# Kernel tuning notes

Hardware: AMD Instinct MI355X
Metric: run time of the kernel (lower is better)

Reference implementation:

```python
import jax, jax.numpy as jnp
import numpy as np

B, S, D, H = 2, 4096, 512, 8
HD = D // H
SCALE = float(np.sqrt(HD))


def setup_inputs() -> dict:
    key = jax.random.key(0)
    ks = jax.random.split(key, 11)
    std = 1.0 / np.sqrt(D)
    inp = {
        "query": jax.random.normal(ks[0], (B, S, D), jnp.float32),
        "key": jax.random.normal(ks[1], (B, S, D), jnp.float32),
        "value": jax.random.normal(ks[2], (B, S, D), jnp.float32),
        "Wq": jax.random.normal(ks[3], (D, D), jnp.float32) * std,
        "bq": jnp.zeros((D,), jnp.float32),
        "Wk": jax.random.normal(ks[4], (D, D), jnp.float32) * std,
        "bk": jnp.zeros((D,), jnp.float32),
        "Wv": jax.random.normal(ks[5], (D, D), jnp.float32) * std,
        "bv": jnp.zeros((D,), jnp.float32),
        "Wo": jax.random.normal(ks[6], (D, D), jnp.float32) * std,
        "bo": jnp.zeros((D,), jnp.float32),
    }
    return inp


def reference(query, key, value, Wq, bq, Wk, bk, Wv, bv, Wo, bo):
    # Linear projections, split into heads: [B, H, S, HD]
    def proj(x, W, b):
        y = jnp.einsum('bsd,df->bsf', x, W) + b
        return y.reshape(B, -1, H, HD).transpose(0, 2, 1, 3)

    Q = proj(query, Wq, bq)
    K = proj(key, Wk, bk)
    V = proj(value, Wv, bv)

    # Full [B, H, S, S] score matrix (faithful to the naive original)
    scores = jnp.einsum('bhqd,bhkd->bhqk', Q, K) / SCALE
    attn = jax.nn.softmax(scores, axis=-1)  # dropout = identity in eval
    attended = jnp.einsum('bhqk,bhkd->bhqd', attn, V)
    attended = attended.transpose(0, 2, 1, 3).reshape(B, -1, D)
    return jnp.einsum('bsd,df->bsf', attended, Wo) + bo
```

## Files before the change

kernel.cpp:

```cpp
#include <hip/hip_runtime.h>

typedef short short8 __attribute__((ext_vector_type(8)));
typedef short short4v __attribute__((ext_vector_type(4)));
typedef float f32x4 __attribute__((ext_vector_type(4)));
typedef float f32x16 __attribute__((ext_vector_type(16)));
typedef unsigned uint2v __attribute__((ext_vector_type(2)));

typedef __attribute__((address_space(1))) void gvoid;
typedef __attribute__((address_space(3))) void lvoid;

#define DEV static __device__ __forceinline__

constexpr int Dm = 512;
constexpr int Sm = 4096;
constexpr int Hh = 8;
constexpr long NTe = (long)2 * Sm * Dm;

#define QSCALE 0.18033688011112042f

DEV short f2bf(float f) {
  union { float f; unsigned u; } v; v.f = f;
  unsigned r = v.u + 0x7FFFu + ((v.u >> 16) & 1u);
  return (short)(r >> 16);
}

DEV float exp2_fast(float x) {
#if __has_builtin(__builtin_amdgcn_exp2f)
  return __builtin_amdgcn_exp2f(x);
#else
  return exp2f(x);
#endif
}

DEV float max3f(float a, float b, float c) { return fmaxf(fmaxf(a, b), c); }

DEV unsigned cvt_pk_bf16(float lo, float hi) {
  unsigned r;
  asm("v_cvt_pk_bf16_f32 %0, %1, %2" : "=v"(r) : "v"(lo), "v"(hi));
  return r;
}

DEV uint2v pl32swap(unsigned a, unsigned b) {
  return __builtin_amdgcn_permlane32_swap(a, b, false, false);
}
DEV float swap_max(float x) { return fmaxf(x, __shfl_xor(x, 32, 64)); }
DEV float swap_add(float x) { return x + __shfl_xor(x, 32, 64); }

DEV void async16(const void* g, void* l) {
  __builtin_amdgcn_global_load_lds((gvoid*)g, (lvoid*)l, 16, 0, 0);
}

__global__ __launch_bounds__(256) void cast_qkv(
    const float* __restrict__ q, const float* __restrict__ k,
    const float* __restrict__ v, short* __restrict__ xq,
    short* __restrict__ xk, short* __restrict__ xv) {
  int t = blockIdx.y;
  const float* src = (t == 0) ? q : (t == 1) ? k : v;
  short* dst = (t == 0) ? xq : (t == 1) ? xk : xv;
  long i = (long)(blockIdx.x * 256 + threadIdx.x) * 4;
  float4 f = *(const float4*)(src + i);
  short4v o;
  o[0] = f2bf(f.x); o[1] = f2bf(f.y); o[2] = f2bf(f.z); o[3] = f2bf(f.w);
  *(short4v*)(dst + i) = o;
}

__global__ __launch_bounds__(256) void wtrans(
    const float* __restrict__ wq, const float* __restrict__ wk,
    const float* __restrict__ wv, const float* __restrict__ wo,
    short* __restrict__ wt) {
  __shared__ short T[64 * 72];
  const int tid = threadIdx.x;
  const int n0 = blockIdx.x * 64, k0 = blockIdx.y * 64, w = blockIdx.z;
  const float* W = (w == 0) ? wq : (w == 1) ? wk : (w == 2) ? wv : wo;
  for (int t = 0; t < 4; ++t) {
    int flat = t * 256 + tid;
    int r = flat >> 4, c4 = flat & 15;
    float4 f = *(const float4*)(W + (k0 + r) * 512 + n0 + c4 * 4);
    T[(c4 * 4 + 0) * 72 + r] = f2bf(f.x);
    T[(c4 * 4 + 1) * 72 + r] = f2bf(f.y);
    T[(c4 * 4 + 2) * 72 + r] = f2bf(f.z);
    T[(c4 * 4 + 3) * 72 + r] = f2bf(f.w);
  }
  __syncthreads();
  for (int t = 0; t < 2; ++t) {
    int flat = t * 256 + tid;
    int r = flat >> 3, c = flat & 7;
    short8 v = *(const short8*)(T + r * 72 + c * 8);
    *(short8*)(wt + ((long)w << 18) + (n0 + r) * 512 + k0 + c * 8) = v;
  }
}

__global__ __launch_bounds__(256) void vtrans(
    const short* __restrict__ V, short* __restrict__ VT) {
  __shared__ short T[64 * 72];
  const int tid = threadIdx.x;
  const int s0 = blockIdx.x * 64, d0 = blockIdx.y * 64, b = blockIdx.z;
  for (int t = 0; t < 2; ++t) {
    int flat = t * 256 + tid;
    int sl = flat >> 3, c = flat & 7;
    short8 v = *(const short8*)(V + ((long)b * Sm + s0 + sl) * Dm + d0 + c * 8);
    for (int j = 0; j < 8; ++j) T[(c * 8 + j) * 72 + sl] = v[j];
  }
  __syncthreads();
  for (int t = 0; t < 2; ++t) {
    int flat = t * 256 + tid;
    int dl = flat >> 3, c = flat & 7;
    short8 v = *(const short8*)(T + dl * 72 + c * 8);
    *(short8*)(VT + ((long)b * Dm + d0 + dl) * Sm + s0 + c * 8) = v;
  }
}

template <bool OUT_BF16>
DEV void gemm_body(const short* __restrict__ A, const short* __restrict__ Bt,
                   const float* __restrict__ bias, float scale,
                   void* __restrict__ Yv, short* As, short* Bs) {
  constexpr int K = 512, N = 512, BK = 64;
  const int tid = threadIdx.x, lane = tid & 63, w = tid >> 6;
  const int lm = lane & 15, lg = lane >> 4;
  const int wr = w >> 1, wc = w & 1;
  const long bm = (long)blockIdx.y * 128;
  const long bn = (long)blockIdx.x * 128;
  f32x4 zero = {0.f, 0.f, 0.f, 0.f};
  f32x4 acc[4][4];
  for (int m = 0; m < 4; ++m)
    for (int n = 0; n < 4; ++n) acc[m][n] = zero;
  for (int k0 = 0; k0 < K; k0 += BK) {
    __syncthreads();
    for (int t = 0; t < 4; ++t) {
      int flat = t * 256 + tid;
      int row = flat >> 3, c = flat & 7;
      async16(A + (bm + row) * K + k0 + ((c ^ (row & 7)) * 8), As + flat * 8);
    }
    for (int t = 0; t < 4; ++t) {
      int flat = t * 256 + tid;
      int row = flat >> 3, c = flat & 7;
      async16(Bt + (bn + row) * K + k0 + ((c ^ (row & 7)) * 8), Bs + flat * 8);
    }
    __syncthreads();
    for (int kk = 0; kk < 2; ++kk) {
      short8 a[4], b[4];
      for (int m = 0; m < 4; ++m)
        a[m] = *(const short8*)(As + (wr * 64 + m * 16 + lm) * BK +
                                ((kk * 4 + lg) ^ (lm & 7)) * 8);
      for (int n = 0; n < 4; ++n)
        b[n] = *(const short8*)(Bs + (wc * 64 + n * 16 + lm) * BK +
                                ((kk * 4 + lg) ^ (lm & 7)) * 8);
      for (int m = 0; m < 4; ++m)
        for (int n = 0; n < 4; ++n)
          acc[m][n] = __builtin_amdgcn_mfma_f32_16x16x32_bf16(a[m], b[n], acc[m][n], 0, 0, 0);
    }
  }
  for (int m = 0; m < 4; ++m)
    for (int n = 0; n < 4; ++n) {
      long row0 = bm + wr * 64 + m * 16 + lg * 4;
      int col = (int)bn + wc * 64 + n * 16 + lm;
      float bb = bias[col];
      for (int j = 0; j < 4; ++j) {
        float val = (acc[m][n][j] + bb) * scale;
        if (OUT_BF16)
          ((short*)Yv)[(row0 + j) * N + col] = f2bf(val);
        else
          ((float*)Yv)[(row0 + j) * N + col] = val;
      }
    }
}

__global__ __launch_bounds__(256) void gemm_proj(
    const short* __restrict__ Xq, const short* __restrict__ Xk,
    const short* __restrict__ Xv, const short* __restrict__ Wt,
    const float* __restrict__ bq, const float* __restrict__ bk,
    const float* __restrict__ bv, short* __restrict__ Qb,
    short* __restrict__ Kb, short* __restrict__ Vb) {
  __shared__ short As[128 * 64];
  __shared__ short Bs[128 * 64];
  int z = blockIdx.z;
  const short* A = (z == 0) ? Xq : (z == 1) ? Xk : Xv;
  const short* Bt = Wt + (long)z * 512 * 512;
  const float* bias = (z == 0) ? bq : (z == 1) ? bk : bv;
  short* Y = (z == 0) ? Qb : (z == 1) ? Kb : Vb;
  float scale = (z == 0) ? QSCALE : 1.f;
  gemm_body<true>(A, Bt, bias, scale, Y, As, Bs);
}

__global__ __launch_bounds__(256) void gemm_out(
    const short* __restrict__ A, const short* __restrict__ Bt,
    const float* __restrict__ bias, float* __restrict__ Y) {
  __shared__ short As[128 * 64];
  __shared__ short Bs[128 * 64];
  gemm_body<false>(A, Bt, bias, 1.f, Y, As, Bs);
}

template <int NSPLIT>
__global__ __launch_bounds__(256) void attn(
    const short* __restrict__ Qb, const short* __restrict__ Kb,
    const short* __restrict__ VTb, float* __restrict__ Op0,
    float* __restrict__ OpRest, float2* __restrict__ Ml) {
  __shared__ short Ks[2][64 * 64];
  __shared__ short Vt[2][64 * 64];
  const int tid = threadIdx.x, lane = tid & 63, w = tid >> 6;
  const int q32 = lane & 31, l5 = lane >> 5;
  const int bh = blockIdx.y, b = bh >> 3, h = bh & 7;
  const int z = blockIdx.z;
  constexpr int KVLEN = Sm / NSPLIT;
  const int kvbase = z * KVLEN;
  const long baseQ = (long)b * Sm * Dm + h * 64;
  const long baseVT = ((long)b * Dm + h * 64) * Sm;
  const int q0w = blockIdx.x * 128 + w * 32;

  short8 qf[4];
#pragma unroll
  for (int ks = 0; ks < 4; ++ks)
    qf[ks] = *(const short8*)(Qb + baseQ + (long)(q0w + q32) * Dm + ks * 16 + l5 * 8);

  f32x16 o0, o1;
#pragma unroll
  for (int r = 0; r < 16; ++r) { o0[r] = 0.f; o1[r] = 0.f; }
  float mrun = -1e30f, lrun = 0.f;

  const int r0 = tid >> 3, c0 = tid & 7;
  const int r1 = 32 + (tid >> 3);
  const short* gk0 = Kb + baseQ + (long)(kvbase + r0) * Dm + (c0 ^ (r0 & 7)) * 8;
  const short* gk1 = Kb + baseQ + (long)(kvbase + r1) * Dm + (c0 ^ (r1 & 7)) * 8;
  const short* gv0 = VTb + baseVT + (long)r0 * Sm + kvbase + (c0 ^ (r0 & 7)) * 8;
  const short* gv1 = VTb + baseVT + (long)r1 * Sm + kvbase + (c0 ^ (r1 & 7)) * 8;
  const int l0 = tid * 8, l1 = (256 + tid) * 8;

  async16(gk0, &Ks[0][l0]); async16(gk1, &Ks[0][l1]);
  async16(gv0, &Vt[0][l0]); async16(gv1, &Vt[0][l1]);
  gk0 += 64 * Dm; gk1 += 64 * Dm; gv0 += 64; gv1 += 64;
  __syncthreads();

  const int cxor = q32 & 7;

  constexpr int NTILES = KVLEN / 64;
  for (int it = 0; it < NTILES; ++it) {
    const int cur = it & 1;
    if (it + 1 < NTILES) {
      async16(gk0, &Ks[cur ^ 1][l0]); async16(gk1, &Ks[cur ^ 1][l1]);
      async16(gv0, &Vt[cur ^ 1][l0]); async16(gv1, &Vt[cur ^ 1][l1]);
      gk0 += 64 * Dm; gk1 += 64 * Dm; gv0 += 64; gv1 += 64;
    }

    f32x16 sc0, sc1;
#pragma unroll
    for (int r = 0; r < 16; ++r) { sc0[r] = 0.f; sc1[r] = 0.f; }
    __builtin_amdgcn_s_setprio(1);
#pragma unroll
    for (int ks = 0; ks < 4; ++ks) {
      int cx = (2 * ks + l5) ^ cxor;
      short8 kf0 = *(const short8*)(&Ks[cur][q32 * 64 + cx * 8]);
      short8 kf1 = *(const short8*)(&Ks[cur][(32 + q32) * 64 + cx * 8]);
      sc0 = __builtin_amdgcn_mfma_f32_32x32x16_bf16(kf0, qf[ks], sc0, 0, 0, 0);
      sc1 = __builtin_amdgcn_mfma_f32_32x32x16_bf16(kf1, qf[ks], sc1, 0, 0, 0);
    }
    __builtin_amdgcn_s_setprio(0);

    float t1 = max3f(sc0[0], sc0[1], sc0[2]);
    float t2 = max3f(sc0[3], sc0[4], sc0[5]);
    float t3 = max3f(sc0[6], sc0[7], sc0[8]);
    float t4 = max3f(sc0[9], sc0[10], sc0[11]);
    float t5 = max3f(sc0[12], sc0[13], sc0[14]);
    float ma = max3f(max3f(t1, t2, t3), max3f(t4, t5, sc0[15]), sc1[0]);
    t1 = max3f(sc1[1], sc1[2], sc1[3]);
    t2 = max3f(sc1[4], sc1[5], sc1[6]);
    t3 = max3f(sc1[7], sc1[8], sc1[9]);
    t4 = max3f(sc1[10], sc1[11], sc1[12]);
    t5 = max3f(sc1[13], sc1[14], sc1[15]);
    float tmax = fmaxf(ma, max3f(max3f(t1, t2, t3), t4, t5));
    tmax = swap_max(tmax);

    if (__any(tmax > mrun + 8.f)) {
      float mi = fmaxf(mrun, tmax);
      float cc = exp2_fast(mrun - mi);
      mrun = mi;
      lrun *= cc;
#pragma unroll
      for (int r = 0; r < 16; ++r) {
        float ccr = __shfl(cc, ((r & 3) + 8 * (r >> 2)) + 4 * l5, 32);
        o0[r] *= ccr;
        o1[r] *= ccr;
      }
    }

    float la = 0.f, lb = 0.f;
#pragma unroll
    for (int r = 0; r < 16; ++r) {
      sc0[r] = exp2_fast(sc0[r] - mrun); la += sc0[r];
      sc1[r] = exp2_fast(sc1[r] - mrun); lb += sc1[r];
    }
    lrun += la + lb;

    __builtin_amdgcn_s_setprio(1);
#pragma unroll
    for (int kc = 0; kc < 4; ++kc) {
      const f32x16& sch = (kc < 2) ? sc0 : sc1;
      const int bb = 8 * (kc & 1);
      unsigned A = cvt_pk_bf16(sch[bb + 0], sch[bb + 1]);
      unsigned B = cvt_pk_bf16(sch[bb + 2], sch[bb + 3]);
      unsigned C = cvt_pk_bf16(sch[bb + 4], sch[bb + 5]);
      unsigned D = cvt_pk_bf16(sch[bb + 6], sch[bb + 7]);
      uint2v rac = pl32swap(A, C);
      uint2v rbd = pl32swap(B, D);
      union { unsigned u[4]; short8 s; } pu;
      pu.u[0] = rac[0]; pu.u[1] = rbd[0]; pu.u[2] = rac[1]; pu.u[3] = rbd[1];
      int cx = (2 * kc + l5) ^ cxor;
      short8 vf0 = *(const short8*)(&Vt[cur][q32 * 64 + cx * 8]);
      short8 vf1 = *(const short8*)(&Vt[cur][(32 + q32) * 64 + cx * 8]);
      o0 = __builtin_amdgcn_mfma_f32_32x32x16_bf16(pu.s, vf0, o0, 0, 0, 0);
      o1 = __builtin_amdgcn_mfma_f32_32x32x16_bf16(pu.s, vf1, o1, 0, 0, 0);
    }
    __builtin_amdgcn_s_setprio(0);
    __syncthreads();
  }

  lrun = swap_add(lrun);

  float* Op = (z == 0) ? Op0 : OpRest + (long)(z - 1) * NTe;
#pragma unroll
  for (int r = 0; r < 16; ++r) {
    int q = (r & 3) + 8 * (r >> 2) + 4 * l5;
    long rowoff = baseQ + (long)(q0w + q) * Dm;
    Op[rowoff + q32] = o0[r];
    Op[rowoff + 32 + q32] = o1[r];
  }
  if (l5 == 0) {
    float2 ml; ml.x = mrun; ml.y = lrun;
    Ml[(long)(z * 16 + bh) * Sm + q0w + q32] = ml;
  }
}

template <int NSPLIT>
__global__ __launch_bounds__(256) void mergeN(
    const float* __restrict__ Op0, const float* __restrict__ OpRest,
    const float2* __restrict__ Ml, short* __restrict__ Ob) {
  long idx = (long)blockIdx.x * 256 + threadIdx.x;
  long row = idx >> 6;
  int c8 = (int)(idx & 63);
  int col = c8 * 8;
  int h = col >> 6;
  int b = (int)(row >> 12);
  int s = (int)(row & 4095);
  int bh = b * 8 + h;
  float2 ml[NSPLIT];
  float M = -3e38f;
#pragma unroll
  for (int z = 0; z < NSPLIT; ++z) {
    ml[z] = Ml[(long)(z * 16 + bh) * Sm + s];
    M = fmaxf(M, ml[z].x);
  }
  float wz[NSPLIT], den = 0.f;
#pragma unroll
  for (int z = 0; z < NSPLIT; ++z) {
    wz[z] = exp2_fast(ml[z].x - M);
    den += ml[z].y * wz[z];
  }
  float inv = 1.0f / den;
  long off = row * 512 + col;
  float acc[8];
#pragma unroll
  for (int i = 0; i < 8; ++i) acc[i] = 0.f;
#pragma unroll
  for (int z = 0; z < NSPLIT; ++z) {
    const float* Op = (z == 0) ? Op0 : OpRest + (long)(z - 1) * NTe;
    float4 a0 = *(const float4*)(Op + off);
    float4 a1 = *(const float4*)(Op + off + 4);
    acc[0] += a0.x * wz[z]; acc[1] += a0.y * wz[z];
    acc[2] += a0.z * wz[z]; acc[3] += a0.w * wz[z];
    acc[4] += a1.x * wz[z]; acc[5] += a1.y * wz[z];
    acc[6] += a1.z * wz[z]; acc[7] += a1.w * wz[z];
  }
  short8 o;
#pragma unroll
  for (int i = 0; i < 8; ++i) o[i] = f2bf(acc[i] * inv);
  *(short8*)(Ob + off) = o;
}

extern "C" void kernel_launch(void* const* d_in, const int* in_sizes, int n_in,
                              void* d_out, int out_size, void* d_ws, size_t ws_size,
                              hipStream_t stream) {
  const float* query = (const float*)d_in[0];
  const float* key_  = (const float*)d_in[1];
  const float* value = (const float*)d_in[2];
  const float* Wq = (const float*)d_in[3]; const float* bq = (const float*)d_in[4];
  const float* Wk = (const float*)d_in[5]; const float* bk = (const float*)d_in[6];
  const float* Wv = (const float*)d_in[7]; const float* bv = (const float*)d_in[8];
  const float* Wo = (const float*)d_in[9]; const float* bo = (const float*)d_in[10];

  short* Xq = (short*)d_ws;
  short* Xk = Xq + NTe;
  short* Xv = Xk + NTe;
  short* Wt = Xv + NTe;
  short* Qb = Wt + 4 * 512 * 512;
  short* Kb = Qb + NTe;
  short* Vb = Kb + NTe;
  short* VT = Xv;
  float* Op0 = (float*)d_ws;
  float* OpRest = (float*)(Vb + NTe);
  short* Ob = Vb;

  const size_t base_bytes = (size_t)(6 * NTe + 4 * 512 * 512) * 2;
  const size_t need4 = base_bytes + 3 * (size_t)NTe * 4 + (size_t)4 * 16 * Sm * 8;
  const int nsplit = (ws_size >= need4) ? 4 : 2;
  float2* Ml = (float2*)(OpRest + (size_t)(nsplit - 1) * NTe);

  cast_qkv<<<dim3(4096, 3), 256, 0, stream>>>(query, key_, value, Xq, Xk, Xv);
  wtrans<<<dim3(8, 8, 4), 256, 0, stream>>>(Wq, Wk, Wv, Wo, Wt);

  gemm_proj<<<dim3(4, 64, 3), 256, 0, stream>>>(Xq, Xk, Xv, Wt, bq, bk, bv,
                                                Qb, Kb, Vb);

  vtrans<<<dim3(Sm / 64, Dm / 64, 2), 256, 0, stream>>>(Vb, VT);

  if (nsplit == 4) {
    attn<4><<<dim3(Sm / 128, 2 * Hh, 4), 256, 0, stream>>>(Qb, Kb, VT, Op0,
                                                           OpRest, Ml);
    mergeN<4><<<dim3((2 * Sm * 512 / 8) / 256), 256, 0, stream>>>(Op0, OpRest,
                                                                  Ml, Ob);
  } else {
    attn<2><<<dim3(Sm / 128, 2 * Hh, 2), 256, 0, stream>>>(Qb, Kb, VT, Op0,
                                                           OpRest, Ml);
    mergeN<2><<<dim3((2 * Sm * 512 / 8) / 256), 256, 0, stream>>>(Op0, OpRest,
                                                                  Ml, Ob);
  }

  gemm_out<<<dim3(4, 64), 256, 0, stream>>>(Ob, Wt + 3L * 512 * 512, bo,
                                            (float*)d_out);
}
```

Before: 184.9 us.

## Store split-KV partials in bf16, widen LDS swizzle, split row-sum accumulators

The attention kernel now writes its unnormalised split-KV partial outputs as bf16 instead of fp32, and the merge kernel reads them back as short8 and converts to float. This halves the partial-output write and read traffic between attention and merge, and shrinks the workspace needed for the 4-way split. It also changes the LDS XOR swizzle to mix bit 3 of the row into the column, aiming to cut bank conflicts in the GEMM and attention tiles. The exp row-sum is split into four partial accumulators to shorten the dependency chain. Rounding the partials to bf16 before the merge adds some numerical error.

```diff
diff --git a/kernel.cpp b/kernel.cpp
--- a/kernel.cpp
+++ b/kernel.cpp
@@ -22,6 +22,12 @@
   union { float f; unsigned u; } v; v.f = f;
   unsigned r = v.u + 0x7FFFu + ((v.u >> 16) & 1u);
   return (short)(r >> 16);
+}
+
+DEV float bf2f(short s) {
+  unsigned u = ((unsigned)(unsigned short)s) << 16;
+  union { unsigned u; float f; } v; v.u = u;
+  return v.f;
 }
 
 DEV float exp2_fast(float x) {
@@ -39,6 +45,8 @@
   asm("v_cvt_pk_bf16_f32 %0, %1, %2" : "=v"(r) : "v"(lo), "v"(hi));
   return r;
 }
+
+DEV int fr(int r) { return (r & 7) ^ (((r >> 3) & 1) << 2); }
 
 DEV uint2v pl32swap(unsigned a, unsigned b) {
   return __builtin_amdgcn_permlane32_swap(a, b, false, false);
@@ -129,22 +137,22 @@
     for (int t = 0; t < 4; ++t) {
       int flat = t * 256 + tid;
       int row = flat >> 3, c = flat & 7;
-      async16(A + (bm + row) * K + k0 + ((c ^ (row & 7)) * 8), As + flat * 8);
+      async16(A + (bm + row) * K + k0 + ((c ^ fr(row)) * 8), As + flat * 8);
     }
     for (int t = 0; t < 4; ++t) {
       int flat = t * 256 + tid;
       int row = flat >> 3, c = flat & 7;
-      async16(Bt + (bn + row) * K + k0 + ((c ^ (row & 7)) * 8), Bs + flat * 8);
+      async16(Bt + (bn + row) * K + k0 + ((c ^ fr(row)) * 8), Bs + flat * 8);
     }
     __syncthreads();
     for (int kk = 0; kk < 2; ++kk) {
       short8 a[4], b[4];
       for (int m = 0; m < 4; ++m)
         a[m] = *(const short8*)(As + (wr * 64 + m * 16 + lm) * BK +
-                                ((kk * 4 + lg) ^ (lm & 7)) * 8);
+                                ((kk * 4 + lg) ^ fr(lm)) * 8);
       for (int n = 0; n < 4; ++n)
         b[n] = *(const short8*)(Bs + (wc * 64 + n * 16 + lm) * BK +
-                                ((kk * 4 + lg) ^ (lm & 7)) * 8);
+                                ((kk * 4 + lg) ^ fr(lm)) * 8);
       for (int m = 0; m < 4; ++m)
         for (int n = 0; n < 4; ++n)
           acc[m][n] = __builtin_amdgcn_mfma_f32_16x16x32_bf16(a[m], b[n], acc[m][n], 0, 0, 0);
@@ -193,8 +201,8 @@
 template <int NSPLIT>
 __global__ __launch_bounds__(256) void attn(
     const short* __restrict__ Qb, const short* __restrict__ Kb,
-    const short* __restrict__ VTb, float* __restrict__ Op0,
-    float* __restrict__ OpRest, float2* __restrict__ Ml) {
+    const short* __restrict__ VTb, short* __restrict__ Op0,
+    short* __restrict__ OpRest, float2* __restrict__ Ml) {
   __shared__ short Ks[2][64 * 64];
   __shared__ short Vt[2][64 * 64];
   const int tid = threadIdx.x, lane = tid & 63, w = tid >> 6;
@@ -219,10 +227,10 @@
 
   const int r0 = tid >> 3, c0 = tid & 7;
   const int r1 = 32 + (tid >> 3);
-  const short* gk0 = Kb + baseQ + (long)(kvbase + r0) * Dm + (c0 ^ (r0 & 7)) * 8;
-  const short* gk1 = Kb + baseQ + (long)(kvbase + r1) * Dm + (c0 ^ (r1 & 7)) * 8;
-  const short* gv0 = VTb + baseVT + (long)r0 * Sm + kvbase + (c0 ^ (r0 & 7)) * 8;
-  const short* gv1 = VTb + baseVT + (long)r1 * Sm + kvbase + (c0 ^ (r1 & 7)) * 8;
+  const short* gk0 = Kb + baseQ + (long)(kvbase + r0) * Dm + (c0 ^ fr(r0)) * 8;
+  const short* gk1 = Kb + baseQ + (long)(kvbase + r1) * Dm + (c0 ^ fr(r1)) * 8;
+  const short* gv0 = VTb + baseVT + (long)r0 * Sm + kvbase + (c0 ^ fr(r0)) * 8;
+  const short* gv1 = VTb + baseVT + (long)r1 * Sm + kvbase + (c0 ^ fr(r1)) * 8;
   const int l0 = tid * 8, l1 = (256 + tid) * 8;
 
   async16(gk0, &Ks[0][l0]); async16(gk1, &Ks[0][l1]);
@@ -230,7 +238,7 @@
   gk0 += 64 * Dm; gk1 += 64 * Dm; gv0 += 64; gv1 += 64;
   __syncthreads();
 
-  const int cxor = q32 & 7;
+  const int cxor = fr(q32);
 
   constexpr int NTILES = KVLEN / 64;
   for (int it = 0; it < NTILES; ++it) {
@@ -282,13 +290,14 @@
       }
     }
 
-    float la = 0.f, lb = 0.f;
+    float la[4] = {0.f, 0.f, 0.f, 0.f}, lb[4] = {0.f, 0.f, 0.f, 0.f};
 #pragma unroll
     for (int r = 0; r < 16; ++r) {
-      sc0[r] = exp2_fast(sc0[r] - mrun); la += sc0[r];
-      sc1[r] = exp2_fast(sc1[r] - mrun); lb += sc1[r];
-    }
-    lrun += la + lb;
+      sc0[r] = exp2_fast(sc0[r] - mrun); la[r & 3] += sc0[r];
+      sc1[r] = exp2_fast(sc1[r] - mrun); lb[r & 3] += sc1[r];
+    }
+    lrun += ((la[0] + la[1]) + (la[2] + la[3])) +
+            ((lb[0] + lb[1]) + (lb[2] + lb[3]));
 
     __builtin_amdgcn_s_setprio(1);
 #pragma unroll
@@ -315,13 +324,13 @@
 
   lrun = swap_add(lrun);
 
-  float* Op = (z == 0) ? Op0 : OpRest + (long)(z - 1) * NTe;
+  short* Op = (z == 0) ? Op0 : OpRest + (long)(z - 1) * NTe;
 #pragma unroll
   for (int r = 0; r < 16; ++r) {
     int q = (r & 3) + 8 * (r >> 2) + 4 * l5;
     long rowoff = baseQ + (long)(q0w + q) * Dm;
-    Op[rowoff + q32] = o0[r];
-    Op[rowoff + 32 + q32] = o1[r];
+    Op[rowoff + q32] = f2bf(o0[r]);
+    Op[rowoff + 32 + q32] = f2bf(o1[r]);
   }
   if (l5 == 0) {
     float2 ml; ml.x = mrun; ml.y = lrun;
@@ -331,7 +340,7 @@
 
 template <int NSPLIT>
 __global__ __launch_bounds__(256) void mergeN(
-    const float* __restrict__ Op0, const float* __restrict__ OpRest,
+    const short* __restrict__ Op0, const short* __restrict__ OpRest,
     const float2* __restrict__ Ml, short* __restrict__ Ob) {
   long idx = (long)blockIdx.x * 256 + threadIdx.x;
   long row = idx >> 6;
@@ -361,13 +370,10 @@
   for (int i = 0; i < 8; ++i) acc[i] = 0.f;
 #pragma unroll
   for (int z = 0; z < NSPLIT; ++z) {
-    const float* Op = (z == 0) ? Op0 : OpRest + (long)(z - 1) * NTe;
-    float4 a0 = *(const float4*)(Op + off);
-    float4 a1 = *(const float4*)(Op + off + 4);
-    acc[0] += a0.x * wz[z]; acc[1] += a0.y * wz[z];
-    acc[2] += a0.z * wz[z]; acc[3] += a0.w * wz[z];
-    acc[4] += a1.x * wz[z]; acc[5] += a1.y * wz[z];
-    acc[6] += a1.z * wz[z]; acc[7] += a1.w * wz[z];
+    const short* Op = (z == 0) ? Op0 : OpRest + (long)(z - 1) * NTe;
+    short8 v = *(const short8*)(Op + off);
+#pragma unroll
+    for (int i = 0; i < 8; ++i) acc[i] += bf2f(v[i]) * wz[z];
   }
   short8 o;
 #pragma unroll
@@ -394,12 +400,12 @@
   short* Kb = Qb + NTe;
   short* Vb = Kb + NTe;
   short* VT = Xv;
-  float* Op0 = (float*)d_ws;
-  float* OpRest = (float*)(Vb + NTe);
+  short* Op0 = Xq;
+  short* OpRest = Vb + NTe;
   short* Ob = Vb;
 
   const size_t base_bytes = (size_t)(6 * NTe + 4 * 512 * 512) * 2;
-  const size_t need4 = base_bytes + 3 * (size_t)NTe * 4 + (size_t)4 * 16 * Sm * 8;
+  const size_t need4 = base_bytes + 3 * (size_t)NTe * 2 + (size_t)4 * 16 * Sm * 8;
   const int nsplit = (ws_size >= need4) ? 4 : 2;
   float2* Ml = (float2*)(OpRest + (size_t)(nsplit - 1) * NTe);
 
```

Result: faster. 179.2 us (-3.1%).
